# Kernel optimization log

Hardware: AMD Instinct MI355X
Metric: run time of the kernel (lower is better)

The kernel has to match this reference:

```python
import jax, jax.numpy as jnp
import numpy as np

GFD = 4096   # global feature dim (VGG fc7)
DH = 1024    # 2 * hidden_dim


def setup_inputs() -> dict:
    key = jax.random.key(0)
    ks = jax.random.split(key, 10)
    b, t_k = 32, 196
    s = lambda fan_in: 1.0 / np.sqrt(fan_in)
    return {
        "global_features": jax.random.normal(ks[0], (b, t_k, GFD), jnp.float32),
        "s_t_hat": jax.random.normal(ks[1], (b, DH), jnp.float32),
        "coverage_img": jnp.zeros((b, t_k, 1), jnp.float32),
        # params
        "Wg": jax.random.normal(ks[2], (GFD, GFD), jnp.float32) * s(GFD),
        "bg": jnp.zeros((GFD,), jnp.float32),
        "Gs": jax.random.normal(ks[3], (GFD, DH), jnp.float32) * s(GFD),
        "bgs": jnp.zeros((DH,), jnp.float32),
        "Wgs": jax.random.normal(ks[4], (DH, DH), jnp.float32) * s(DH),  # w_g_star, no bias
        "Wdec": jax.random.normal(ks[5], (DH, DH), jnp.float32) * s(DH),  # decode_proj
        "bdec": jnp.zeros((DH,), jnp.float32),
        "v": jax.random.normal(ks[6], (DH, 1), jnp.float32) * s(DH),  # score vector, no bias
    }


def reference(global_features, s_t_hat, coverage_img, Wg, bg, Gs, bgs, Wgs, Wdec, bdec, v):
    # g_star: project 4096-d region features -> 1024-d   [b, t_k, DH]
    g1 = global_features @ Wg + bg
    g_star = g1 @ Gs + bgs
    # additive (Bahdanau) scores with coverage
    w_g_star = g_star @ Wgs                       # [b, t_k, DH]
    dec_fea = s_t_hat @ Wdec + bdec               # [b, DH]
    e_a = jnp.tanh(w_g_star + dec_fea[:, None, :] + coverage_img)  # [b, t_k, DH]
    scores = e_a @ v                              # [b, t_k, 1]
    alpha_a = jax.nn.softmax(scores, axis=1)      # softmax over regions
    # attention-weighted context (the bmm)
    c_img = jnp.einsum("bt,btd->bd", alpha_a[..., 0], g_star)  # [b, DH]
    coverage_new = coverage_img + alpha_a
    return c_img, coverage_new, alpha_a
```

## Files before the change

### kernel.cpp

```cpp
#include <hip/hip_runtime.h>
#include <hip/hip_bf16.h>

typedef __attribute__((ext_vector_type(8))) short short8;
typedef __attribute__((ext_vector_type(4))) float floatx4;

#define GLOBAL_AS __attribute__((address_space(1)))
#define LDS_AS    __attribute__((address_space(3)))

__device__ __forceinline__ unsigned short f2bf_rne(float x) {
  unsigned int u = __float_as_uint(x);
  u += 0x7fffu + ((u >> 16) & 1u);
  return (unsigned short)(u >> 16);
}

__global__ void cast_f32_bf16_kernel(const float* __restrict__ in,
                                     unsigned short* __restrict__ out, int n8) {
  int i = blockIdx.x * 256 + threadIdx.x;
  if (i >= n8) return;
  const float4* p = (const float4*)in;
  float4 v0 = p[2 * i], v1 = p[2 * i + 1];
  short8 o;
  o[0] = (short)f2bf_rne(v0.x); o[1] = (short)f2bf_rne(v0.y);
  o[2] = (short)f2bf_rne(v0.z); o[3] = (short)f2bf_rne(v0.w);
  o[4] = (short)f2bf_rne(v1.x); o[5] = (short)f2bf_rne(v1.y);
  o[6] = (short)f2bf_rne(v1.z); o[7] = (short)f2bf_rne(v1.w);
  *(short8*)(out + 8 * (size_t)i) = o;
}

__global__ void transpose_cast_kernel(const float* __restrict__ in,
                                      unsigned short* __restrict__ out, int R, int C) {
  __shared__ unsigned short tile[32][33];
  int tx = threadIdx.x & 31, ty = threadIdx.x >> 5;
  int r0 = blockIdx.y * 32, c0 = blockIdx.x * 32;
#pragma unroll
  for (int j = 0; j < 32; j += 8)
    tile[ty + j][tx] = f2bf_rne(in[(size_t)(r0 + ty + j) * C + c0 + tx]);
  __syncthreads();
#pragma unroll
  for (int j = 0; j < 32; j += 8)
    out[(size_t)(c0 + ty + j) * R + r0 + tx] = tile[tx][ty + j];
}

__global__ void zero4_kernel(float* __restrict__ p, int n4) {
  int i = blockIdx.x * 256 + threadIdx.x;
  if (i < n4) ((float4*)p)[i] = make_float4(0.f, 0.f, 0.f, 0.f);
}
__global__ void init_vec_kernel(const float* __restrict__ src, float* __restrict__ dst) {
  int i = blockIdx.x * 256 + threadIdx.x;
  dst[i] = src[i];
}
__global__ void bias1_accum_kernel(const float* __restrict__ bg, const float* __restrict__ Gs,
                                   float* __restrict__ bias1) {
  int j = blockIdx.x * 256 + threadIdx.x;
  int k0 = blockIdx.y * 256;
  float acc = 0.f;
  for (int k = 0; k < 256; ++k) acc += bg[k0 + k] * Gs[(size_t)(k0 + k) * 1024 + j];
  atomicAdd(&bias1[j], acc);
}

__global__ void init_dec_kernel(const float* __restrict__ bdec, float* __restrict__ dec) {
  int i = blockIdx.x * 256 + threadIdx.x;
  dec[i] = bdec[i & 1023];
}
__global__ void dec_accum_kernel(const float* __restrict__ sth, const float* __restrict__ Wdec,
                                 float* __restrict__ dec) {
  __shared__ float ss[32][128];
  const int tid = threadIdx.x;
  const int k0 = blockIdx.y * 128;
  for (int i = tid; i < 32 * 128; i += 256) {
    int bb = i >> 7, kk = i & 127;
    ss[bb][kk] = sth[bb * 1024 + k0 + kk];
  }
  __syncthreads();
  const int j = blockIdx.x * 256 + tid;
  float acc[32];
#pragma unroll
  for (int b = 0; b < 32; ++b) acc[b] = 0.f;
  for (int kk = 0; kk < 128; ++kk) {
    float w = Wdec[(size_t)(k0 + kk) * 1024 + j];
#pragma unroll
    for (int b = 0; b < 32; ++b) acc[b] += ss[b][kk] * w;
  }
  for (int b = 0; b < 32; ++b) atomicAdd(&dec[b * 1024 + j], acc[b]);
}

template <int BM, int BN, bool HAS_BIAS, bool WRITE_F32, bool WRITE_BF16>
__global__ __launch_bounds__(256, 4) void gemm_tile_kernel(
    const unsigned short* __restrict__ A, const unsigned short* __restrict__ BT,
    const float* __restrict__ bias, float* __restrict__ Cf,
    unsigned short* __restrict__ Cb, int M, int N, int K) {
  constexpr int AF = BM / 32;
  constexpr int BF = BN / 32;
  constexpr int ASLAB = BM * 64;
  constexpr int BSLAB = BN * 64;
  __shared__ unsigned short lds_a[BM * 64];
  __shared__ unsigned short lds_b[BN * 64];
  const int tid = threadIdx.x;
  const int lane = tid & 63;
  const int wave = tid >> 6;
  const int wm = wave >> 1, wn = wave & 1;
  const int quad = lane >> 4, col = lane & 15;
  const int m0 = blockIdx.y * BM, n0 = blockIdx.x * BN;

  floatx4 acc[AF][BF] = {};

  const int srow = tid >> 2;
  const int skoff = (tid & 3) * 8;
  const unsigned short* a_ptr = A + (size_t)(m0 + srow) * K + skoff;
  const unsigned short* b_ptr = BT + (size_t)(n0 + srow) * K + skoff;
  const size_t rowskip = (size_t)64 * K;
  char* la_dst = (char*)lds_a + tid * 16;
  char* lb_dst = (char*)lds_b + tid * 16;

  for (int kt = 0; kt < K; kt += 64) {
    __syncthreads();
#pragma unroll
    for (int h = 0; h < BM / 64; ++h)
#pragma unroll
      for (int s = 0; s < 2; ++s)
        __builtin_amdgcn_global_load_lds((const GLOBAL_AS void*)(a_ptr + h * rowskip + s * 32),
                                         (LDS_AS void*)(la_dst + s * ASLAB + h * 4096), 16, 0, 0);
#pragma unroll
    for (int h = 0; h < BN / 64; ++h)
#pragma unroll
      for (int s = 0; s < 2; ++s)
        __builtin_amdgcn_global_load_lds((const GLOBAL_AS void*)(b_ptr + h * rowskip + s * 32),
                                         (LDS_AS void*)(lb_dst + s * BSLAB + h * 4096), 16, 0, 0);
    a_ptr += 64; b_ptr += 64;
    __syncthreads();
#pragma unroll
    for (int s = 0; s < 2; ++s) {
      short8 af[AF], bf[BF];
#pragma unroll
      for (int t = 0; t < AF; ++t)
        af[t] = *(const short8*)((const char*)lds_a + s * ASLAB +
                                 (wm * (BM / 2) + t * 16 + col) * 64 + quad * 16);
#pragma unroll
      for (int t = 0; t < BF; ++t)
        bf[t] = *(const short8*)((const char*)lds_b + s * BSLAB +
                                 (wn * (BN / 2) + t * 16 + col) * 64 + quad * 16);
#pragma unroll
      for (int tm = 0; tm < AF; ++tm)
#pragma unroll
        for (int tn = 0; tn < BF; ++tn)
          acc[tm][tn] = __builtin_amdgcn_mfma_f32_16x16x32_bf16(af[tm], bf[tn], acc[tm][tn], 0, 0, 0);
    }
  }

#pragma unroll
  for (int tm = 0; tm < AF; ++tm) {
    const int mg = m0 + wm * (BM / 2) + tm * 16 + quad * 4;
#pragma unroll
    for (int tn = 0; tn < BF; ++tn) {
      const int ng = n0 + wn * (BN / 2) + tn * 16 + col;
      const float bv = HAS_BIAS ? bias[ng] : 0.0f;
#pragma unroll
      for (int r = 0; r < 4; ++r) {
        const float val = acc[tm][tn][r] + bv;
        if (WRITE_F32) Cf[(size_t)(mg + r) * N + ng] = val;
        if (WRITE_BF16) Cb[(size_t)(mg + r) * N + ng] = f2bf_rne(val);
      }
    }
  }
}

__global__ __launch_bounds__(256, 4) void gemm_scores_kernel(
    const unsigned short* __restrict__ A, const unsigned short* __restrict__ BT,
    const float* __restrict__ dec, const float* __restrict__ cov,
    const float* __restrict__ v, float* __restrict__ scores, int M, int N, int K) {
  __shared__ unsigned short lds_a[128 * 64];
  __shared__ unsigned short lds_b[64 * 64];
  const int tid = threadIdx.x;
  const int lane = tid & 63;
  const int wave = tid >> 6;
  const int wm = wave >> 1, wn = wave & 1;
  const int quad = lane >> 4, col = lane & 15;
  const int m0 = blockIdx.y * 128, n0 = blockIdx.x * 64;

  floatx4 acc[4][2] = {};

  const int srow = tid >> 2;
  const int skoff = (tid & 3) * 8;
  const unsigned short* a_ptr = A + (size_t)(m0 + srow) * K + skoff;
  const unsigned short* b_ptr = BT + (size_t)(n0 + srow) * K + skoff;
  const size_t rowskip = (size_t)64 * K;
  char* la_dst = (char*)lds_a + tid * 16;
  char* lb_dst = (char*)lds_b + tid * 16;

  for (int kt = 0; kt < K; kt += 64) {
    __syncthreads();
#pragma unroll
    for (int h = 0; h < 2; ++h)
#pragma unroll
      for (int s = 0; s < 2; ++s)
        __builtin_amdgcn_global_load_lds((const GLOBAL_AS void*)(a_ptr + h * rowskip + s * 32),
                                         (LDS_AS void*)(la_dst + s * 8192 + h * 4096), 16, 0, 0);
#pragma unroll
    for (int s = 0; s < 2; ++s)
      __builtin_amdgcn_global_load_lds((const GLOBAL_AS void*)(b_ptr + s * 32),
                                       (LDS_AS void*)(lb_dst + s * 4096), 16, 0, 0);
    a_ptr += 64; b_ptr += 64;
    __syncthreads();
#pragma unroll
    for (int s = 0; s < 2; ++s) {
      short8 af[4], bf[2];
#pragma unroll
      for (int t = 0; t < 4; ++t)
        af[t] = *(const short8*)((const char*)lds_a + s * 8192 +
                                 (wm * 64 + t * 16 + col) * 64 + quad * 16);
#pragma unroll
      for (int t = 0; t < 2; ++t)
        bf[t] = *(const short8*)((const char*)lds_b + s * 4096 +
                                 (wn * 32 + t * 16 + col) * 64 + quad * 16);
#pragma unroll
      for (int tm = 0; tm < 4; ++tm)
#pragma unroll
        for (int tn = 0; tn < 2; ++tn)
          acc[tm][tn] = __builtin_amdgcn_mfma_f32_16x16x32_bf16(af[tm], bf[tn], acc[tm][tn], 0, 0, 0);
    }
  }

  const int n_base = n0 + wn * 32;
  float vv[2];
#pragma unroll
  for (int tn = 0; tn < 2; ++tn) vv[tn] = v[n_base + tn * 16 + col];
#pragma unroll
  for (int tm = 0; tm < 4; ++tm) {
#pragma unroll
    for (int r = 0; r < 4; ++r) {
      const int row = m0 + wm * 64 + tm * 16 + quad * 4 + r;
      const int b = row / 196;
      const float cw = cov[row];
      const float* dr = dec + b * 1024 + n_base;
      float s = 0.f;
#pragma unroll
      for (int tn = 0; tn < 2; ++tn)
        s += tanhf(acc[tm][tn][r] + dr[tn * 16 + col] + cw) * vv[tn];
      s += __shfl_xor(s, 1, 64);
      s += __shfl_xor(s, 2, 64);
      s += __shfl_xor(s, 4, 64);
      s += __shfl_xor(s, 8, 64);
      if ((lane & 15) == 0) atomicAdd(&scores[row], s);
    }
  }
}

__global__ void softmax_kernel(const float* __restrict__ scores, const float* __restrict__ cov,
                               float* __restrict__ alpha_ws, float* __restrict__ out) {
  const int b = blockIdx.x, tid = threadIdx.x;
  const int lane = tid & 63, wid = tid >> 6;
  __shared__ float red[8];
  float s = (tid < 196) ? scores[b * 196 + tid] : -1e30f;
  float m = s;
  for (int off = 32; off > 0; off >>= 1) m = fmaxf(m, __shfl_xor(m, off, 64));
  if (lane == 0) red[wid] = m;
  __syncthreads();
  m = fmaxf(fmaxf(red[0], red[1]), fmaxf(red[2], red[3]));
  float e = (tid < 196) ? __expf(s - m) : 0.f;
  float t = e;
  for (int off = 32; off > 0; off >>= 1) t += __shfl_xor(t, off, 64);
  if (lane == 0) red[4 + wid] = t;
  __syncthreads();
  const float tot = red[4] + red[5] + red[6] + red[7];
  const float a = e / tot;
  if (tid < 196) {
    alpha_ws[b * 196 + tid] = a;
    out[32768 + b * 196 + tid] = cov[b * 196 + tid] + a;
    out[32768 + 6272 + b * 196 + tid] = a;
  }
}

__global__ __launch_bounds__(256) void ctx_kernel(const float* __restrict__ alpha,
                                                  const float* __restrict__ gstar,
                                                  float* __restrict__ out) {
  const int b = blockIdx.y;
  const int colbase = blockIdx.x * 128;
  const int c = threadIdx.x & 127;
  const int half = threadIdx.x >> 7;
  const float* g = gstar + ((size_t)b * 196 + half * 98) * 1024 + colbase + c;
  const float* al = alpha + b * 196 + half * 98;
  float acc = 0.f;
#pragma unroll 7
  for (int t = 0; t < 98; ++t) acc += al[t] * g[(size_t)t * 1024];
  __shared__ float part[256];
  part[threadIdx.x] = acc;
  __syncthreads();
  if (threadIdx.x < 128)
    out[b * 1024 + colbase + threadIdx.x] = part[threadIdx.x] + part[threadIdx.x + 128];
}

extern "C" void kernel_launch(void* const* d_in, const int* in_sizes, int n_in,
                              void* d_out, int out_size, void* d_ws, size_t ws_size,
                              hipStream_t stream) {
  (void)in_sizes; (void)n_in; (void)out_size; (void)ws_size;
  const float* gf   = (const float*)d_in[0];
  const float* sth  = (const float*)d_in[1];
  const float* cov  = (const float*)d_in[2];
  const float* Wg   = (const float*)d_in[3];
  const float* bg   = (const float*)d_in[4];
  const float* Gs   = (const float*)d_in[5];
  const float* bgs  = (const float*)d_in[6];
  const float* Wgs  = (const float*)d_in[7];
  const float* Wdec = (const float*)d_in[8];
  const float* bdec = (const float*)d_in[9];
  const float* v    = (const float*)d_in[10];
  float* out = (float*)d_out;

  char* ws = (char*)d_ws;
  unsigned short* gf_bf   = (unsigned short*)(ws + 0);
  float*          alpha   = (float*)(ws + 0);
  unsigned short* Wg_bf   = (unsigned short*)(ws + 51380224);
  float*          gstar_f = (float*)(ws + 51380224);
  unsigned short* GsT     = (unsigned short*)(ws + 84934656);
  unsigned short* WgsT    = (unsigned short*)(ws + 84934656);
  unsigned short* C1T_b   = (unsigned short*)(ws + 93323264);
  unsigned short* gstar_b = (unsigned short*)(ws + 101711872);
  float*          bias1   = (float*)(ws + 114556928);
  float*          dec     = (float*)(ws + 114561024);
  float*          scores  = (float*)(ws + 114692096);

  cast_f32_bf16_kernel<<<12544, 256, 0, stream>>>(gf, gf_bf, 3211264);
  cast_f32_bf16_kernel<<<8192, 256, 0, stream>>>(Wg, Wg_bf, 2097152);
  transpose_cast_kernel<<<dim3(32, 128), 256, 0, stream>>>(Gs, GsT, 4096, 1024);
  init_vec_kernel<<<4, 256, 0, stream>>>(bgs, bias1);
  bias1_accum_kernel<<<dim3(4, 16), 256, 0, stream>>>(bg, Gs, bias1);
  gemm_tile_kernel<128, 64, false, false, true><<<dim3(64, 8), 256, 0, stream>>>(
      GsT, Wg_bf, nullptr, nullptr, C1T_b, 1024, 4096, 4096);
  transpose_cast_kernel<<<dim3(32, 32), 256, 0, stream>>>(Wgs, WgsT, 1024, 1024);
  init_dec_kernel<<<128, 256, 0, stream>>>(bdec, dec);
  dec_accum_kernel<<<dim3(4, 8), 256, 0, stream>>>(sth, Wdec, dec);
  gemm_tile_kernel<128, 64, true, true, true><<<dim3(16, 49), 256, 0, stream>>>(
      gf_bf, C1T_b, bias1, gstar_f, gstar_b, 6272, 1024, 4096);
  zero4_kernel<<<2, 256, 0, stream>>>(scores, 392);
  gemm_scores_kernel<<<dim3(16, 49), 256, 0, stream>>>(
      gstar_b, WgsT, dec, cov, v, scores, 6272, 1024, 1024);
  softmax_kernel<<<32, 256, 0, stream>>>(scores, cov, alpha, out);
  ctx_kernel<<<dim3(8, 32), 256, 0, stream>>>(alpha, gstar_f, out);
}
```

Before: 503.9 us.

## Double-buffer LDS tiles in GEMMs, swizzle block order, enlarge main GEMM tile

Both MFMA GEMM kernels now double-buffer their LDS tiles, issuing the next K-tile's global-to-LDS loads before computing on the current one, with a single barrier per iteration. Block IDs are remapped with an XCD-style swizzle (stride by eight) so neighbouring tiles land on the same die and share L2, and the first GEMM's grid is transposed. The large projection GEMM moves from 128x64 to 128x128 tiles, and launch bounds drop to two blocks per CU to fit the doubled LDS. The aim is to hide global load latency and cut redundant operand reads, at the cost of lower occupancy and more registers per thread.

```diff
diff --git a/kernel.cpp b/kernel.cpp
--- a/kernel.cpp
+++ b/kernel.cpp
@@ -84,8 +84,8 @@
   for (int b = 0; b < 32; ++b) atomicAdd(&dec[b * 1024 + j], acc[b]);
 }
 
-template <int BM, int BN, bool HAS_BIAS, bool WRITE_F32, bool WRITE_BF16>
-__global__ __launch_bounds__(256, 4) void gemm_tile_kernel(
+template <int BM, int BN, bool HAS_BIAS, bool WRITE_F32, bool WRITE_BF16, bool SWAPXY>
+__global__ __launch_bounds__(256, 2) void gemm_tile_kernel(
     const unsigned short* __restrict__ A, const unsigned short* __restrict__ BT,
     const float* __restrict__ bias, float* __restrict__ Cf,
     unsigned short* __restrict__ Cb, int M, int N, int K) {
@@ -93,14 +93,23 @@
   constexpr int BF = BN / 32;
   constexpr int ASLAB = BM * 64;
   constexpr int BSLAB = BN * 64;
-  __shared__ unsigned short lds_a[BM * 64];
-  __shared__ unsigned short lds_b[BN * 64];
+  constexpr int ABUF = 2 * ASLAB;
+  constexpr int BBUF = 2 * BSLAB;
+  __shared__ unsigned short lds_a[BM * 128];
+  __shared__ unsigned short lds_b[BN * 128];
   const int tid = threadIdx.x;
   const int lane = tid & 63;
   const int wave = tid >> 6;
   const int wm = wave >> 1, wn = wave & 1;
   const int quad = lane >> 4, col = lane & 15;
-  const int m0 = blockIdx.y * BM, n0 = blockIdx.x * BN;
+
+  const int gx = (int)gridDim.x;
+  const int nwg = gx * (int)gridDim.y;
+  const int bid = (int)blockIdx.y * gx + (int)blockIdx.x;
+  const int swz = (bid & 7) * (nwg >> 3) + (bid >> 3);
+  const int bx = swz % gx, by = swz / gx;
+  const int m0 = (SWAPXY ? bx : by) * BM;
+  const int n0 = (SWAPXY ? by : bx) * BN;
 
   floatx4 acc[AF][BF] = {};
 
@@ -109,42 +118,63 @@
   const unsigned short* a_ptr = A + (size_t)(m0 + srow) * K + skoff;
   const unsigned short* b_ptr = BT + (size_t)(n0 + srow) * K + skoff;
   const size_t rowskip = (size_t)64 * K;
-  char* la_dst = (char*)lds_a + tid * 16;
-  char* lb_dst = (char*)lds_b + tid * 16;
-
-  for (int kt = 0; kt < K; kt += 64) {
-    __syncthreads();
-#pragma unroll
-    for (int h = 0; h < BM / 64; ++h)
-#pragma unroll
-      for (int s = 0; s < 2; ++s)
-        __builtin_amdgcn_global_load_lds((const GLOBAL_AS void*)(a_ptr + h * rowskip + s * 32),
-                                         (LDS_AS void*)(la_dst + s * ASLAB + h * 4096), 16, 0, 0);
-#pragma unroll
-    for (int h = 0; h < BN / 64; ++h)
-#pragma unroll
-      for (int s = 0; s < 2; ++s)
-        __builtin_amdgcn_global_load_lds((const GLOBAL_AS void*)(b_ptr + h * rowskip + s * 32),
-                                         (LDS_AS void*)(lb_dst + s * BSLAB + h * 4096), 16, 0, 0);
-    a_ptr += 64; b_ptr += 64;
-    __syncthreads();
+  char* const la_dst = (char*)lds_a + tid * 16;
+  char* const lb_dst = (char*)lds_b + tid * 16;
+
+#pragma unroll
+  for (int h = 0; h < BM / 64; ++h)
+#pragma unroll
+    for (int s = 0; s < 2; ++s)
+      __builtin_amdgcn_global_load_lds((const GLOBAL_AS void*)(a_ptr + h * rowskip + s * 32),
+                                       (LDS_AS void*)(la_dst + s * ASLAB + h * 4096), 16, 0, 0);
+#pragma unroll
+  for (int h = 0; h < BN / 64; ++h)
+#pragma unroll
+    for (int s = 0; s < 2; ++s)
+      __builtin_amdgcn_global_load_lds((const GLOBAL_AS void*)(b_ptr + h * rowskip + s * 32),
+                                       (LDS_AS void*)(lb_dst + s * BSLAB + h * 4096), 16, 0, 0);
+  a_ptr += 64; b_ptr += 64;
+  __syncthreads();
+
+  const int NT = K >> 6;
+  int cur = 0;
+  for (int t = 0; t < NT; ++t) {
+    if (t + 1 < NT) {
+      char* la = la_dst + (cur ^ 1) * ABUF;
+      char* lb = lb_dst + (cur ^ 1) * BBUF;
+#pragma unroll
+      for (int h = 0; h < BM / 64; ++h)
+#pragma unroll
+        for (int s = 0; s < 2; ++s)
+          __builtin_amdgcn_global_load_lds((const GLOBAL_AS void*)(a_ptr + h * rowskip + s * 32),
+                                           (LDS_AS void*)(la + s * ASLAB + h * 4096), 16, 0, 0);
+#pragma unroll
+      for (int h = 0; h < BN / 64; ++h)
+#pragma unroll
+        for (int s = 0; s < 2; ++s)
+          __builtin_amdgcn_global_load_lds((const GLOBAL_AS void*)(b_ptr + h * rowskip + s * 32),
+                                           (LDS_AS void*)(lb + s * BSLAB + h * 4096), 16, 0, 0);
+      a_ptr += 64; b_ptr += 64;
+    }
+    const char* pa = (const char*)lds_a + cur * ABUF;
+    const char* pb = (const char*)lds_b + cur * BBUF;
 #pragma unroll
     for (int s = 0; s < 2; ++s) {
       short8 af[AF], bf[BF];
 #pragma unroll
-      for (int t = 0; t < AF; ++t)
-        af[t] = *(const short8*)((const char*)lds_a + s * ASLAB +
-                                 (wm * (BM / 2) + t * 16 + col) * 64 + quad * 16);
-#pragma unroll
-      for (int t = 0; t < BF; ++t)
-        bf[t] = *(const short8*)((const char*)lds_b + s * BSLAB +
-                                 (wn * (BN / 2) + t * 16 + col) * 64 + quad * 16);
+      for (int tf = 0; tf < AF; ++tf)
+        af[tf] = *(const short8*)(pa + s * ASLAB + (wm * (BM / 2) + tf * 16 + col) * 64 + quad * 16);
+#pragma unroll
+      for (int tf = 0; tf < BF; ++tf)
+        bf[tf] = *(const short8*)(pb + s * BSLAB + (wn * (BN / 2) + tf * 16 + col) * 64 + quad * 16);
 #pragma unroll
       for (int tm = 0; tm < AF; ++tm)
 #pragma unroll
         for (int tn = 0; tn < BF; ++tn)
           acc[tm][tn] = __builtin_amdgcn_mfma_f32_16x16x32_bf16(af[tm], bf[tn], acc[tm][tn], 0, 0, 0);
     }
+    __syncthreads();
+    cur ^= 1;
   }
 
 #pragma unroll
@@ -164,18 +194,25 @@
   }
 }
 
-__global__ __launch_bounds__(256, 4) void gemm_scores_kernel(
+__global__ __launch_bounds__(256, 2) void gemm_scores_kernel(
     const unsigned short* __restrict__ A, const unsigned short* __restrict__ BT,
     const float* __restrict__ dec, const float* __restrict__ cov,
     const float* __restrict__ v, float* __restrict__ scores, int M, int N, int K) {
-  __shared__ unsigned short lds_a[128 * 64];
-  __shared__ unsigned short lds_b[64 * 64];
+  constexpr int ASLAB = 8192, ABUF = 16384;
+  constexpr int BSLAB = 4096, BBUF = 8192;
+  __shared__ unsigned short lds_a[128 * 128];
+  __shared__ unsigned short lds_b[64 * 128];
   const int tid = threadIdx.x;
   const int lane = tid & 63;
   const int wave = tid >> 6;
   const int wm = wave >> 1, wn = wave & 1;
   const int quad = lane >> 4, col = lane & 15;
-  const int m0 = blockIdx.y * 128, n0 = blockIdx.x * 64;
+
+  const int gx = (int)gridDim.x;
+  const int nwg = gx * (int)gridDim.y;
+  const int bid = (int)blockIdx.y * gx + (int)blockIdx.x;
+  const int swz = (bid & 7) * (nwg >> 3) + (bid >> 3);
+  const int m0 = (swz / gx) * 128, n0 = (swz % gx) * 64;
 
   floatx4 acc[4][2] = {};
 
@@ -184,40 +221,59 @@
   const unsigned short* a_ptr = A + (size_t)(m0 + srow) * K + skoff;
   const unsigned short* b_ptr = BT + (size_t)(n0 + srow) * K + skoff;
   const size_t rowskip = (size_t)64 * K;
-  char* la_dst = (char*)lds_a + tid * 16;
-  char* lb_dst = (char*)lds_b + tid * 16;
-
-  for (int kt = 0; kt < K; kt += 64) {
-    __syncthreads();
-#pragma unroll
-    for (int h = 0; h < 2; ++h)
+  char* const la_dst = (char*)lds_a + tid * 16;
+  char* const lb_dst = (char*)lds_b + tid * 16;
+
+#pragma unroll
+  for (int h = 0; h < 2; ++h)
+#pragma unroll
+    for (int s = 0; s < 2; ++s)
+      __builtin_amdgcn_global_load_lds((const GLOBAL_AS void*)(a_ptr + h * rowskip + s * 32),
+                                       (LDS_AS void*)(la_dst + s * ASLAB + h * 4096), 16, 0, 0);
+#pragma unroll
+  for (int s = 0; s < 2; ++s)
+    __builtin_amdgcn_global_load_lds((const GLOBAL_AS void*)(b_ptr + s * 32),
+                                     (LDS_AS void*)(lb_dst + s * BSLAB), 16, 0, 0);
+  a_ptr += 64; b_ptr += 64;
+  __syncthreads();
+
+  const int NT = K >> 6;
+  int cur = 0;
+  for (int t = 0; t < NT; ++t) {
+    if (t + 1 < NT) {
+      char* la = la_dst + (cur ^ 1) * ABUF;
+      char* lb = lb_dst + (cur ^ 1) * BBUF;
+#pragma unroll
+      for (int h = 0; h < 2; ++h)
+#pragma unroll
+        for (int s = 0; s < 2; ++s)
+          __builtin_amdgcn_global_load_lds((const GLOBAL_AS void*)(a_ptr + h * rowskip + s * 32),
+                                           (LDS_AS void*)(la + s * ASLAB + h * 4096), 16, 0, 0);
 #pragma unroll
       for (int s = 0; s < 2; ++s)
-        __builtin_amdgcn_global_load_lds((const GLOBAL_AS void*)(a_ptr + h * rowskip + s * 32),
-                                         (LDS_AS void*)(la_dst + s * 8192 + h * 4096), 16, 0, 0);
-#pragma unroll
-    for (int s = 0; s < 2; ++s)
-      __builtin_amdgcn_global_load_lds((const GLOBAL_AS void*)(b_ptr + s * 32),
-                                       (LDS_AS void*)(lb_dst + s * 4096), 16, 0, 0);
-    a_ptr += 64; b_ptr += 64;
-    __syncthreads();
+        __builtin_amdgcn_global_load_lds((const GLOBAL_AS void*)(b_ptr + s * 32),
+                                         (LDS_AS void*)(lb + s * BSLAB), 16, 0, 0);
+      a_ptr += 64; b_ptr += 64;
+    }
+    const char* pa = (const char*)lds_a + cur * ABUF;
+    const char* pb = (const char*)lds_b + cur * BBUF;
 #pragma unroll
     for (int s = 0; s < 2; ++s) {
       short8 af[4], bf[2];
 #pragma unroll
-      for (int t = 0; t < 4; ++t)
-        af[t] = *(const short8*)((const char*)lds_a + s * 8192 +
-                                 (wm * 64 + t * 16 + col) * 64 + quad * 16);
-#pragma unroll
-      for (int t = 0; t < 2; ++t)
-        bf[t] = *(const short8*)((const char*)lds_b + s * 4096 +
-                                 (wn * 32 + t * 16 + col) * 64 + quad * 16);
+      for (int tf = 0; tf < 4; ++tf)
+        af[tf] = *(const short8*)(pa + s * ASLAB + (wm * 64 + tf * 16 + col) * 64 + quad * 16);
+#pragma unroll
+      for (int tf = 0; tf < 2; ++tf)
+        bf[tf] = *(const short8*)(pb + s * BSLAB + (wn * 32 + tf * 16 + col) * 64 + quad * 16);
 #pragma unroll
       for (int tm = 0; tm < 4; ++tm)
 #pragma unroll
         for (int tn = 0; tn < 2; ++tn)
           acc[tm][tn] = __builtin_amdgcn_mfma_f32_16x16x32_bf16(af[tm], bf[tn], acc[tm][tn], 0, 0, 0);
     }
+    __syncthreads();
+    cur ^= 1;
   }
 
   const int n_base = n0 + wn * 32;
@@ -324,12 +380,12 @@
   transpose_cast_kernel<<<dim3(32, 128), 256, 0, stream>>>(Gs, GsT, 4096, 1024);
   init_vec_kernel<<<4, 256, 0, stream>>>(bgs, bias1);
   bias1_accum_kernel<<<dim3(4, 16), 256, 0, stream>>>(bg, Gs, bias1);
-  gemm_tile_kernel<128, 64, false, false, true><<<dim3(64, 8), 256, 0, stream>>>(
+  gemm_tile_kernel<128, 64, false, false, true, true><<<dim3(8, 64), 256, 0, stream>>>(
       GsT, Wg_bf, nullptr, nullptr, C1T_b, 1024, 4096, 4096);
   transpose_cast_kernel<<<dim3(32, 32), 256, 0, stream>>>(Wgs, WgsT, 1024, 1024);
   init_dec_kernel<<<128, 256, 0, stream>>>(bdec, dec);
   dec_accum_kernel<<<dim3(4, 8), 256, 0, stream>>>(sth, Wdec, dec);
-  gemm_tile_kernel<128, 64, true, true, true><<<dim3(16, 49), 256, 0, stream>>>(
+  gemm_tile_kernel<128, 128, true, true, true, false><<<dim3(8, 49), 256, 0, stream>>>(
       gf_bf, C1T_b, bias1, gstar_f, gstar_b, 6272, 1024, 4096);
   zero4_kernel<<<2, 256, 0, stream>>>(scores, 392);
   gemm_scores_kernel<<<dim3(16, 49), 256, 0, stream>>>(
```

After: 505.7 us. No clear change (+0.4%).
